# Optimization experiments

Hardware: AMD Instinct MI355X
Metric: run time of the kernel (lower is better)

Reference implementation:

```python
import jax, jax.numpy as jnp
import numpy as np

EMBED_DIM = 1024
NUM_HEADS = 16
HEAD_DIM = EMBED_DIM // NUM_HEADS
SEG_LENS = [1024, 2048, 4096]
DIL_RATIOS = [1, 2, 4]
NEG = -1e8  # lse fill value used by sparse_to_dense


def setup_inputs() -> dict:
    root = jax.random.key(0)
    ks = jax.random.split(root, 12)
    B, L, E = 1, 4096, EMBED_DIM
    s = 0.02
    return {
        "query": jax.random.normal(ks[0], (B, L, E), jnp.float32),
        "key": jax.random.normal(ks[1], (B, L, E), jnp.float32),
        "value": jax.random.normal(ks[2], (B, L, E), jnp.float32),
        "Wq": jax.random.normal(ks[3], (E, E), jnp.float32) * s,
        "bq": jnp.zeros((E,), jnp.float32),
        "Wk": jax.random.normal(ks[4], (E, E), jnp.float32) * s,
        "bk": jnp.zeros((E,), jnp.float32),
        "Wv": jax.random.normal(ks[5], (E, E), jnp.float32) * s,
        "bv": jnp.zeros((E,), jnp.float32),
        "Wo": jax.random.normal(ks[6], (E, E), jnp.float32) * s,
        "bo": jnp.zeros((E,), jnp.float32),
    }


def _branch(q, k, v, sl, dr, L):
    """One (segment_length, dilated_ratio) branch.
    q,k,v: (B, L, H, D). Returns dense out (B, H, L, D) and lse (B, H, L).
    """
    B = q.shape[0]
    H, D = NUM_HEADS, HEAD_DIM
    sl = min(sl, L)
    pad = (-L) % sl
    if pad:
        pw = ((0, 0), (0, pad), (0, 0), (0, 0))
        q, k, v = jnp.pad(q, pw), jnp.pad(k, pw), jnp.pad(v, pw)
    n = (L + pad) // sl  # segments
    qs = q.reshape(B * n, sl, H, D)
    ks = k.reshape(B * n, sl, H, D)
    vs = v.reshape(B * n, sl, H, D)
    # dense_to_sparse: head j (group r = j // (H//dr)) keeps positions i*dr + r
    hg = H // dr
    g = sl // dr
    grp = jnp.arange(H) // hg                      # (H,)
    pos = jnp.arange(g)[:, None] * dr + grp[None]  # (g, H) dense positions
    hidx = jnp.arange(H)[None, :]
    sp = lambda x: x[:, pos, hidx, :]              # (B*n, g, H, D)
    qd, kd, vd = sp(qs), sp(ks), sp(vs)
    # causal attention within each sparse segment (flash_attn semantics)
    scores = jnp.einsum('bqhd,bkhd->bhqk', qd, kd) * (D ** -0.5)
    mask = jnp.tril(jnp.ones((g, g), bool))
    scores = jnp.where(mask, scores, -jnp.inf)
    lse = jax.nn.logsumexp(scores, axis=-1)        # (B*n, H, g)
    o = jnp.einsum('bhqk,bkhd->bqhd', jnp.exp(scores - lse[..., None]), vd)
    # sparse_to_dense: scatter back onto dense positions, NEG elsewhere
    hcol = jnp.arange(H)[:, None]                  # (H,1)
    od = jnp.zeros((B * n, H, sl, D), o.dtype).at[:, hcol, pos.T].set(
        o.transpose(0, 2, 1, 3))
    ld = jnp.zeros((B * n, H, sl), lse.dtype).at[:, hcol, pos.T].set(lse)
    ld = jnp.where(ld == 0.0, NEG, ld)  # matches masked_fill_(lse == 0, -1e8)
    od = od.reshape(B, n, H, sl, D).transpose(0, 2, 1, 3, 4)
    od = od.reshape(B, H, n * sl, D)[:, :, :L]
    ld = ld.reshape(B, n, H, sl).transpose(0, 2, 1, 3).reshape(B, H, n * sl)[:, :, :L]
    return od, ld


def reference(query, key, value, Wq, bq, Wk, bk, Wv, bv, Wo, bo):
    B, L, E = query.shape
    H, D = NUM_HEADS, HEAD_DIM
    q = (query @ Wq.T + bq).reshape(B, L, H, D)
    k = (key @ Wk.T + bk).reshape(B, L, H, D)
    v = (value @ Wv.T + bv).reshape(B, L, H, D)
    outs, lses = [], []
    for sl, dr in zip(SEG_LENS, DIL_RATIOS):
        o, l = _branch(q, k, v, sl, dr, L)
        outs.append(o)
        lses.append(l)
    lse_all = jnp.stack(lses, 0)[..., None]        # (nb, B, H, L, 1)
    m = lse_all.max(0)
    w = jnp.exp(lse_all - m)
    w = w / w.sum(0)                               # softmax merge weights
    w = jax.lax.stop_gradient(w)                   # torch computes under no_grad
    out = sum(o * wi.astype(o.dtype) for o, wi in zip(outs, w))  # (B,H,L,D)
    out = out.transpose(0, 2, 1, 3).reshape(B, L, E)
    return out @ Wo.T + bo
```

## Files before the change

kernel.cpp:

```cpp
#include <hip/hip_runtime.h>
#include <math.h>


#define L_SEQ 4096
#define EDIM  1024
#define NH    16
#define HD    64
#define GLEN  1024

typedef __bf16 bf16;
typedef __bf16 bf16x8 __attribute__((ext_vector_type(8)));
typedef __bf16 bf16x4 __attribute__((ext_vector_type(4)));
typedef short  s16x4  __attribute__((ext_vector_type(4)));
typedef float  f32x4  __attribute__((ext_vector_type(4)));

template <bool B> struct Flag { static constexpr bool v = B; };

__device__ __forceinline__ void gload16(const bf16* g, bf16* l) {
  __builtin_amdgcn_global_load_lds(
      (__attribute__((address_space(1))) void*)(const_cast<bf16*>(g)),
      (__attribute__((address_space(3))) void*)(l),
      16, 0, 0);
}

__device__ __forceinline__ f32x4 mfma16x16x16_bf16(bf16x4 a, bf16x4 b, f32x4 c) {
#if defined(__HIP_DEVICE_COMPILE__)
  union { bf16x4 h; s16x4 s; } ua, ub;
  ua.h = a; ub.h = b;
  return __builtin_amdgcn_mfma_f32_16x16x16bf16_1k(ua.s, ub.s, c, 0, 0, 0);
#else
  (void)a; (void)b;
  return c;
#endif
}

__device__ __forceinline__ float fast_exp2(float x) {
#if __has_builtin(__builtin_amdgcn_exp2f)
  return __builtin_amdgcn_exp2f(x);
#else
  return __expf(x * 0.6931471805599453f);
#endif
}

__global__ __launch_bounds__(256) void cvt_kernel(
    const float* q, const float* k, const float* v,
    const float* wq, const float* wk, const float* wv, const float* wo,
    bf16* oq, bf16* ok, bf16* ov,
    bf16* owq, bf16* owk, bf16* owv, bf16* owo)
{
  const float* src; bf16* dst; int n;
  switch (blockIdx.y) {
    case 0: src = q;  dst = oq;  n = L_SEQ*EDIM; break;
    case 1: src = k;  dst = ok;  n = L_SEQ*EDIM; break;
    case 2: src = v;  dst = ov;  n = L_SEQ*EDIM; break;
    case 3: src = wq; dst = owq; n = EDIM*EDIM; break;
    case 4: src = wk; dst = owk; n = EDIM*EDIM; break;
    case 5: src = wv; dst = owv; n = EDIM*EDIM; break;
    default: src = wo; dst = owo; n = EDIM*EDIM; break;
  }
  int i = (blockIdx.x * 256 + threadIdx.x) * 8;
  if (i >= n) return;
  const float4* s4 = (const float4*)(src + i);
  float4 a = s4[0], b = s4[1];
  bf16x8 o = { (bf16)a.x, (bf16)a.y, (bf16)a.z, (bf16)a.w,
               (bf16)b.x, (bf16)b.y, (bf16)b.z, (bf16)b.w };
  *(bf16x8*)(dst + i) = o;
}

template <typename OutT>
__device__ __forceinline__ void gemm_body(const bf16* __restrict__ A,
                                          const bf16* __restrict__ W,
                                          const float* __restrict__ bias,
                                          OutT* __restrict__ C)
{
  constexpr int K = 1024;
  __shared__ __align__(16) bf16 lA[128 * 32];
  __shared__ __align__(16) bf16 lB[128 * 32];

  const int tid  = threadIdx.x;
  const int lane = tid & 63;
  const int w    = tid >> 6;
  const int quad = lane >> 4;
  const int l16  = lane & 15;
  const int wr   = w >> 1, wc = w & 1;
  const int ly = blockIdx.x * 4 + (blockIdx.y >> 3);
  const int lx = blockIdx.y & 7;
  const int row0 = ly * 128;
  const int col0 = lx * 128;

  f32x4 acc[4][4] = {};

  const int c0 = tid, c1 = tid + 256;
  const bf16* Ab0 = A + (size_t)(row0 + (c0 >> 2)) * K + (c0 & 3) * 8;
  const bf16* Ab1 = A + (size_t)(row0 + (c1 >> 2)) * K + (c1 & 3) * 8;
  const bf16* Bb0 = W + (size_t)(col0 + (c0 >> 2)) * K + (c0 & 3) * 8;
  const bf16* Bb1 = W + (size_t)(col0 + (c1 >> 2)) * K + (c1 & 3) * 8;
  bf16* lA0 = &lA[c0 * 8]; bf16* lA1 = &lA[c1 * 8];
  bf16* lB0 = &lB[c0 * 8]; bf16* lB1 = &lB[c1 * 8];

  for (int kt = 0; kt < K; kt += 32) {
    __syncthreads();
    gload16(Ab0 + kt, lA0);
    gload16(Ab1 + kt, lA1);
    gload16(Bb0 + kt, lB0);
    gload16(Bb1 + kt, lB1);
    __syncthreads();

    bf16x8 af[4], bfrag[4];
#pragma unroll
    for (int mi = 0; mi < 4; mi++)
      af[mi] = *(const bf16x8*)&lA[(wr * 64 + mi * 16 + l16) * 32 + quad * 8];
#pragma unroll
    for (int ni = 0; ni < 4; ni++)
      bfrag[ni] = *(const bf16x8*)&lB[(wc * 64 + ni * 16 + l16) * 32 + quad * 8];
#pragma unroll
    for (int mi = 0; mi < 4; mi++)
#pragma unroll
      for (int ni = 0; ni < 4; ni++)
        acc[mi][ni] = __builtin_amdgcn_mfma_f32_16x16x32_bf16(
            af[mi], bfrag[ni], acc[mi][ni], 0, 0, 0);
  }

#pragma unroll
  for (int mi = 0; mi < 4; mi++) {
#pragma unroll
    for (int ni = 0; ni < 4; ni++) {
      const int gcol = col0 + wc * 64 + ni * 16 + l16;
      const float bv = bias[gcol];
#pragma unroll
      for (int r = 0; r < 4; r++) {
        const int grow = row0 + wr * 64 + mi * 16 + quad * 4 + r;
        C[(size_t)grow * 1024 + gcol] = (OutT)(acc[mi][ni][r] + bv);
      }
    }
  }
}

__global__ __launch_bounds__(256) void gemm_qkv_kernel(
    const bf16* xq, const bf16* xk, const bf16* xv,
    const bf16* wq, const bf16* wk, const bf16* wv,
    const float* bq, const float* bk, const float* bv,
    bf16* q, bf16* k, bf16* v)
{
  const bf16 *A, *W; const float* bias; bf16* C;
  if (blockIdx.z == 0)      { A = xq; W = wq; bias = bq; C = q; }
  else if (blockIdx.z == 1) { A = xk; W = wk; bias = bk; C = k; }
  else                      { A = xv; W = wv; bias = bv; C = v; }
  gemm_body<bf16>(A, W, bias, C);
}

__global__ __launch_bounds__(256) void gemm_out_kernel(
    const bf16* A, const bf16* W, const float* bias, float* C)
{
  gemm_body<float>(A, W, bias, C);
}

__global__ __launch_bounds__(256) void vtrans_kernel(
    const bf16* __restrict__ v, bf16* vt0, bf16* vt1, bf16* vt2)
{
  __shared__ __align__(16) bf16 ltile[64 * 72];
  const int bid = blockIdx.x;
  int sl, dr, rem, shift; bf16* vt;
  if (bid < 1024)      { sl = 1024; dr = 1; rem = bid;        vt = vt0; shift = 4; }
  else if (bid < 1536) { sl = 2048; dr = 2; rem = bid - 1024; vt = vt1; shift = 3; }
  else                 { sl = 4096; dr = 4; rem = bid - 1536; vt = vt2; shift = 2; }
  const int ktile = rem & 15;
  const int h     = (rem >> 4) & 15;
  const int seg   = rem >> 8;
  const int grp   = h >> shift;
  const int segbase = seg * sl;
  const int tid = threadIdx.x;
  {
    const int i = tid >> 2, dc = tid & 3;
    const size_t p = (size_t)(segbase + (ktile * 64 + i) * dr + grp);
    const bf16* src = v + p * EDIM + h * 64 + dc * 16;
    *(uint4*)&ltile[i * 72 + dc * 16]     = *(const uint4*)(src);
    *(uint4*)&ltile[i * 72 + dc * 16 + 8] = *(const uint4*)(src + 8);
  }
  __syncthreads();
  {
    const int d = tid >> 2, kc = tid & 3;
    __align__(16) bf16 tmp[16];
#pragma unroll
    for (int j = 0; j < 16; j++) tmp[j] = ltile[(kc * 16 + j) * 72 + d];
    const int p2 = kc >> 1, half = kc & 1;
    bf16* dst = vt + ((size_t)(seg * NH + h) * 64 + d) * GLEN + ktile * 64
                   + p2 * 32 + half * 4;
#pragma unroll
    for (int q = 0; q < 4; q++) {
      bf16x4 piece = { tmp[q * 4 + 0], tmp[q * 4 + 1],
                       tmp[q * 4 + 2], tmp[q * 4 + 3] };
      *(bf16x4*)(dst + q * 8) = piece;
    }
  }
}

__global__ __launch_bounds__(256, 4) void attn_kernel(
    const bf16* __restrict__ qg, const bf16* __restrict__ kg,
    const bf16* vt0, const bf16* vt1, const bf16* vt2,
    bf16* o0, bf16* o1, bf16* o2,
    float* l0, float* l1, float* l2)
{
  __shared__ __align__(16) bf16 lK[2][64 * 64];
  __shared__ __align__(16) bf16 lV[2][64 * 64];

  const int bid0 = blockIdx.x;
  const int o = (bid0 & 7) * 112 + (bid0 >> 3);

  int sl, dr, rem, shift;
  const bf16* vt; bf16* ob; float* lseb;
  if (o < 512)      { sl = 1024; dr = 1; rem = o;       vt = vt0; ob = o0; lseb = l0; shift = 4; }
  else if (o < 768) { sl = 2048; dr = 2; rem = o - 512; vt = vt1; ob = o1; lseb = l1; shift = 3; }
  else              { sl = 4096; dr = 4; rem = o - 768; vt = vt2; ob = o2; lseb = l2; shift = 2; }
  const int j   = rem & 7;
  const int h   = (rem >> 3) & 15;
  const int seg = rem >> 7;
  const int qtA = 15 - j;
  const int qtB = j;
  const int grp = h >> shift;
  const int segbase = seg * sl;

  const int tid = threadIdx.x, lane = tid & 63, w = tid >> 6;
  const int quad = lane >> 4, l16 = lane & 15;
  const int rs8 = l16 & 7;

  auto loadq = [&](int qt, bf16x8& a0, bf16x8& a1) {
    const int qi = qt * 64 + w * 16 + l16;
    const size_t p = (size_t)(segbase + qi * dr + grp);
    const bf16* qp = qg + p * EDIM + h * 64 + quad * 8;
    a0 = *(const bf16x8*)(qp);
    a1 = *(const bf16x8*)(qp + 32);
  };
  bf16x8 qaA0, qaA1, qaB0, qaB1;
  loadq(qtA, qaA0, qaA1);
  loadq(qtB, qaB0, qaB1);

  f32x4 OA[4] = {}, OB[4] = {};
  float mA = -__builtin_inff(), lA_ = 0.f;
  float mB = -__builtin_inff(), lB_ = 0.f;

  const bf16* vbase = vt + (size_t)(seg * NH + h) * 64 * GLEN;
  const int c0 = tid, c1 = tid + 256;
  const int r0 = c0 >> 3, sw0 = ((c0 & 7) ^ (r0 & 7));
  const int r1 = c1 >> 3, sw1 = ((c1 & 7) ^ (r1 & 7));

  const bf16* kp0 = kg + (size_t)(segbase + r0 * dr + grp) * EDIM + h * 64 + sw0 * 8;
  const bf16* kp1 = kg + (size_t)(segbase + r1 * dr + grp) * EDIM + h * 64 + sw1 * 8;
  const bf16* vp0 = vbase + (size_t)r0 * GLEN + sw0 * 8;
  const bf16* vp1 = vbase + (size_t)r1 * GLEN + sw1 * 8;
  const size_t kstep = (size_t)64 * dr * EDIM;

  auto stage = [&](int buf) {
    gload16(kp0, &lK[buf][c0 * 8]);
    gload16(kp1, &lK[buf][c1 * 8]);
    gload16(vp0, &lV[buf][c0 * 8]);
    gload16(vp1, &lV[buf][c1 * 8]);
    kp0 += kstep; kp1 += kstep; vp0 += 64; vp1 += 64;
  };

  const float CS = 0.18033688011112042f;
  const float NEGINF = -__builtin_inff();
  const int qiA = qtA * 64 + w * 16 + l16;
  const int qiB = qtB * 64 + w * 16 + l16;

  const int kb0 = l16 * 64 + ((quad ^ rs8) * 8);
  const int kb1 = l16 * 64 + (((4 + quad) ^ rs8) * 8);
  const int vb0 = l16 * 64;

  auto comp = [&](auto hasB_, auto diagA_, auto diagB_, int kt) {
    constexpr bool HAS_B  = decltype(hasB_)::v;
    constexpr bool DIAG_A = decltype(diagA_)::v;
    constexpr bool DIAG_B = decltype(diagB_)::v;
    const bf16* bK = lK[kt & 1];
    const bf16* bV = lV[kt & 1];

    f32x4 sA[4], sB[4];
    __builtin_amdgcn_s_setprio(1);
#pragma unroll
    for (int t = 0; t < 4; t++) {
      const bool aA = !DIAG_A || t <= w;
      const bool aB = HAS_B && (!DIAG_B || t <= w);
      if (aA || aB) {
        bf16x8 ka0 = *(const bf16x8*)&bK[kb0 + t * 1024];
        bf16x8 ka1 = *(const bf16x8*)&bK[kb1 + t * 1024];
        if (aA) {
          sA[t] = f32x4{0.f, 0.f, 0.f, 0.f};
          sA[t] = __builtin_amdgcn_mfma_f32_16x16x32_bf16(ka0, qaA0, sA[t], 0, 0, 0);
          sA[t] = __builtin_amdgcn_mfma_f32_16x16x32_bf16(ka1, qaA1, sA[t], 0, 0, 0);
        }
        if (aB) {
          sB[t] = f32x4{0.f, 0.f, 0.f, 0.f};
          sB[t] = __builtin_amdgcn_mfma_f32_16x16x32_bf16(ka0, qaB0, sB[t], 0, 0, 0);
          sB[t] = __builtin_amdgcn_mfma_f32_16x16x32_bf16(ka1, qaB1, sB[t], 0, 0, 0);
        }
      }
    }
    __builtin_amdgcn_s_setprio(0);

    f32x4 mvA = {NEGINF, NEGINF, NEGINF, NEGINF};
    f32x4 mvB = {NEGINF, NEGINF, NEGINF, NEGINF};
#pragma unroll
    for (int t = 0; t < 4; t++) {
      if (!DIAG_A || t <= w) {
#pragma unroll
        for (int r = 0; r < 4; r++) {
          float sv = sA[t][r];
          if (DIAG_A) {
            const int kj = kt * 64 + t * 16 + quad * 4 + r;
            if (kj > qiA) sv = NEGINF;
          }
          sA[t][r] = sv;
          mvA[r] = fmaxf(mvA[r], sv);
        }
      }
      if (HAS_B && (!DIAG_B || t <= w)) {
#pragma unroll
        for (int r = 0; r < 4; r++) {
          float sv = sB[t][r];
          if (DIAG_B) {
            const int kj = kt * 64 + t * 16 + quad * 4 + r;
            if (kj > qiB) sv = NEGINF;
          }
          sB[t][r] = sv;
          mvB[r] = fmaxf(mvB[r], sv);
        }
      }
    }
    float mrA = fmaxf(fmaxf(mvA[0], mvA[1]), fmaxf(mvA[2], mvA[3]));
    float mrB = fmaxf(fmaxf(mvB[0], mvB[1]), fmaxf(mvB[2], mvB[3]));
    mrA = fmaxf(mrA, __shfl_xor(mrA, 16, 64));
    mrA = fmaxf(mrA, __shfl_xor(mrA, 32, 64));
    if constexpr (HAS_B) {
      mrB = fmaxf(mrB, __shfl_xor(mrB, 16, 64));
      mrB = fmaxf(mrB, __shfl_xor(mrB, 32, 64));
    }

    {
      const float mnew = fmaxf(mA, mrA * CS);
      if (!__all(mnew - mA <= 8.0f)) {
        const float alpha = fast_exp2(mA - mnew);
#pragma unroll
        for (int nf = 0; nf < 4; nf++)
#pragma unroll
          for (int r = 0; r < 4; r++) OA[nf][r] *= alpha;
        lA_ *= alpha;
        mA = mnew;
      }
    }
    if constexpr (HAS_B) {
      const float mnew = fmaxf(mB, mrB * CS);
      if (!__all(mnew - mB <= 8.0f)) {
        const float alpha = fast_exp2(mB - mnew);
#pragma unroll
        for (int nf = 0; nf < 4; nf++)
#pragma unroll
          for (int r = 0; r < 4; r++) OB[nf][r] *= alpha;
        lB_ *= alpha;
        mB = mnew;
      }
    }

    bf16x4 pbA[4], pbB[4];
    f32x4 rvA = {0.f, 0.f, 0.f, 0.f}, rvB = {0.f, 0.f, 0.f, 0.f};
#pragma unroll
    for (int t = 0; t < 4; t++) {
      if (!DIAG_A || t <= w) {
#pragma unroll
        for (int r = 0; r < 4; r++) {
          const float pv = fast_exp2(__builtin_fmaf(sA[t][r], CS, -mA));
          pbA[t][r] = (bf16)pv;
          rvA[r] += pv;
        }
      }
      if (HAS_B && (!DIAG_B || t <= w)) {
#pragma unroll
        for (int r = 0; r < 4; r++) {
          const float pv = fast_exp2(__builtin_fmaf(sB[t][r], CS, -mB));
          pbB[t][r] = (bf16)pv;
          rvB[r] += pv;
        }
      }
    }
    float rsA = (rvA[0] + rvA[1]) + (rvA[2] + rvA[3]);
    rsA += __shfl_xor(rsA, 16, 64);
    rsA += __shfl_xor(rsA, 32, 64);
    lA_ += rsA;
    if constexpr (HAS_B) {
      float rsB = (rvB[0] + rvB[1]) + (rvB[2] + rvB[3]);
      rsB += __shfl_xor(rsB, 16, 64);
      rsB += __shfl_xor(rsB, 32, 64);
      lB_ += rsB;
    }

    __builtin_amdgcn_s_setprio(1);
#pragma unroll
    for (int p2 = 0; p2 < 2; p2++) {
      const int t0 = 2 * p2, t1 = t0 + 1;
      const bool aA0 = !DIAG_A || t0 <= w;
      const bool aA1 = !DIAG_A || t1 <= w;
      const bool aB0 = HAS_B && (!DIAG_B || t0 <= w);
      const bool aB1 = HAS_B && (!DIAG_B || t1 <= w);
      if (aA0 || aA1 || aB0 || aB1) {
        const int cx = ((p2 * 4 + quad) ^ rs8) * 8;
#pragma unroll
        for (int nf = 0; nf < 4; nf++) {
          bf16x8 va8 = *(const bf16x8*)&bV[vb0 + nf * 1024 + cx];
          bf16x4 vlo = __builtin_shufflevector(va8, va8, 0, 1, 2, 3);
          bf16x4 vhi = __builtin_shufflevector(va8, va8, 4, 5, 6, 7);
          if (aA0) OA[nf] = mfma16x16x16_bf16(vlo, pbA[t0], OA[nf]);
          if (aA1) OA[nf] = mfma16x16x16_bf16(vhi, pbA[t1], OA[nf]);
          if (aB0) OB[nf] = mfma16x16x16_bf16(vlo, pbB[t0], OB[nf]);
          if (aB1) OB[nf] = mfma16x16x16_bf16(vhi, pbB[t1], OB[nf]);
        }
      }
    }
    __builtin_amdgcn_s_setprio(0);
  };

  stage(0);
  int kt = 0;
  for (; kt < qtB; kt++) {
    __syncthreads();
    stage((kt + 1) & 1);
    comp(Flag<true>{}, Flag<false>{}, Flag<false>{}, kt);
  }
  __syncthreads();
  stage((kt + 1) & 1);
  comp(Flag<true>{}, Flag<false>{}, Flag<true>{}, kt);
  kt++;
  for (; kt < qtA; kt++) {
    __syncthreads();
    stage((kt + 1) & 1);
    comp(Flag<false>{}, Flag<false>{}, Flag<false>{}, kt);
  }
  __syncthreads();
  comp(Flag<false>{}, Flag<true>{}, Flag<false>{}, kt);

  auto epilogue = [&](const f32x4 (&Oa)[4], float m_r, float l_r, int qt) {
    const int qi = qt * 64 + w * 16 + l16;
    const float linv = 1.0f / l_r;
    const int pdense = segbase + qi * dr + grp;
    bf16* orow = ob + (size_t)pdense * EDIM + h * 64;
#pragma unroll
    for (int nf = 0; nf < 4; nf++) {
      bf16x4 ov;
#pragma unroll
      for (int r = 0; r < 4; r++) ov[r] = (bf16)(Oa[nf][r] * linv);
      *(bf16x4*)(orow + nf * 16 + quad * 4) = ov;
    }
    if (quad == 0)
      lseb[h * L_SEQ + pdense] = m_r * 0.6931471805599453f + __logf(l_r);
  };
  epilogue(OA, mA, lA_, qtA);
  epilogue(OB, mB, lB_, qtB);
}

__global__ __launch_bounds__(256) void merge_kernel(
    const bf16* __restrict__ o0, const bf16* __restrict__ o1, const bf16* __restrict__ o2,
    const float* __restrict__ l0, const float* __restrict__ l1, const float* __restrict__ l2,
    bf16* __restrict__ merged)
{
  const int idx = blockIdx.x * 256 + threadIdx.x;
  const int dc = idx & 7;
  const int h  = (idx >> 3) & 15;
  const int p  = idx >> 7;
  const bool c1 = ((p & 1) == (h >> 3));
  const bool c2 = ((p & 3) == (h >> 2));
  const float s0 = l0[h * L_SEQ + p];
  const float s1 = c1 ? l1[h * L_SEQ + p] : -__builtin_inff();
  const float s2 = c2 ? l2[h * L_SEQ + p] : -__builtin_inff();
  const float mx = fmaxf(s0, fmaxf(s1, s2));
  float w0 = __expf(s0 - mx);
  float w1 = c1 ? __expf(s1 - mx) : 0.f;
  float w2 = c2 ? __expf(s2 - mx) : 0.f;
  const float inv = 1.0f / (w0 + w1 + w2);
  w0 *= inv; w1 *= inv; w2 *= inv;

  const size_t off = (size_t)p * EDIM + h * 64 + dc * 8;
  float acc[8];
  bf16x8 a0 = *(const bf16x8*)(o0 + off);
#pragma unroll
  for (int j = 0; j < 8; j++) acc[j] = w0 * (float)a0[j];
  if (c1) {
    bf16x8 a1 = *(const bf16x8*)(o1 + off);
#pragma unroll
    for (int j = 0; j < 8; j++) acc[j] += w1 * (float)a1[j];
  }
  if (c2) {
    bf16x8 a2 = *(const bf16x8*)(o2 + off);
#pragma unroll
    for (int j = 0; j < 8; j++) acc[j] += w2 * (float)a2[j];
  }
  bf16x8 r;
#pragma unroll
  for (int j = 0; j < 8; j++) r[j] = (bf16)acc[j];
  *(bf16x8*)(merged + off) = r;
}

extern "C" void kernel_launch(void* const* d_in, const int* in_sizes, int n_in,
                              void* d_out, int out_size, void* d_ws, size_t ws_size,
                              hipStream_t stream)
{
  (void)in_sizes; (void)n_in; (void)out_size; (void)ws_size;
  const float* query = (const float*)d_in[0];
  const float* key   = (const float*)d_in[1];
  const float* value = (const float*)d_in[2];
  const float* Wq = (const float*)d_in[3];
  const float* bq = (const float*)d_in[4];
  const float* Wk = (const float*)d_in[5];
  const float* bk = (const float*)d_in[6];
  const float* Wv = (const float*)d_in[7];
  const float* bv = (const float*)d_in[8];
  const float* Wo = (const float*)d_in[9];
  const float* bo = (const float*)d_in[10];

  char* base = (char*)d_ws;
  size_t off = 0;
  auto take = [&](size_t nbytes) -> char* {
    char* p = base + off;
    off += (nbytes + 255) & ~(size_t)255;
    return p;
  };
  const size_t LE2 = (size_t)L_SEQ * EDIM * 2;
  const size_t EE2 = (size_t)EDIM * EDIM * 2;
  bf16* xq  = (bf16*)take(LE2);
  bf16* xk  = (bf16*)take(LE2);
  bf16* xv  = (bf16*)take(LE2);
  bf16* wqb = (bf16*)take(EE2);
  bf16* wkb = (bf16*)take(EE2);
  bf16* wvb = (bf16*)take(EE2);
  bf16* wob = (bf16*)take(EE2);
  bf16* qb  = (bf16*)take(LE2);
  bf16* kb  = (bf16*)take(LE2);
  bf16* vb  = (bf16*)take(LE2);
  bf16* vt0 = (bf16*)take((size_t)4 * NH * HD * GLEN * 2);
  bf16* vt1 = (bf16*)take((size_t)2 * NH * HD * GLEN * 2);
  bf16* vt2 = (bf16*)take((size_t)1 * NH * HD * GLEN * 2);
  float* lse0 = (float*)take((size_t)NH * L_SEQ * 4);
  float* lse1 = (float*)take((size_t)NH * L_SEQ * 4);
  float* lse2 = (float*)take((size_t)NH * L_SEQ * 4);
  bf16* merged = (bf16*)take(LE2);
  bf16* o0 = xq; bf16* o1 = xk; bf16* o2 = xv;

  dim3 blk(256);
  cvt_kernel<<<dim3(2048, 7), blk, 0, stream>>>(
      query, key, value, Wq, Wk, Wv, Wo, xq, xk, xv, wqb, wkb, wvb, wob);
  gemm_qkv_kernel<<<dim3(8, 32, 3), blk, 0, stream>>>(
      xq, xk, xv, wqb, wkb, wvb, bq, bk, bv, qb, kb, vb);
  vtrans_kernel<<<dim3(1792), blk, 0, stream>>>(vb, vt0, vt1, vt2);
  attn_kernel<<<dim3(896), blk, 0, stream>>>(
      qb, kb, vt0, vt1, vt2, o0, o1, o2, lse0, lse1, lse2);
  merge_kernel<<<dim3(2048), blk, 0, stream>>>(
      o0, o1, o2, lse0, lse1, lse2, merged);
  gemm_out_kernel<<<dim3(8, 32), blk, 0, stream>>>(merged, wob, bo, (float*)d_out);
}
```

Measured before the change: 227.2 us.

## Fuse fp32-to-bf16 activation conversion into QKV GEMM and compute row sums via MFMA

The QKV GEMM now reads fp32 activations directly, converting them to bf16 in registers and prefetching the next K-tile into registers before writing it to LDS. This removes the separate conversion pass over the three large input tensors and its bf16 round trip through memory. In the attention kernel, the softmax row-sum is accumulated with an MFMA against a ones vector instead of VALU adds and cross-lane shuffles. The s_setprio hints are also removed. The trade-off is extra MFMA issue in attention, and in the GEMM a register-staged A path that replaces the async global-to-LDS load.

```diff
diff --git a/kernel.cpp b/kernel.cpp
--- a/kernel.cpp
+++ b/kernel.cpp
@@ -43,23 +43,17 @@
 }
 
 __global__ __launch_bounds__(256) void cvt_kernel(
-    const float* q, const float* k, const float* v,
     const float* wq, const float* wk, const float* wv, const float* wo,
-    bf16* oq, bf16* ok, bf16* ov,
     bf16* owq, bf16* owk, bf16* owv, bf16* owo)
 {
-  const float* src; bf16* dst; int n;
+  const float* src; bf16* dst;
   switch (blockIdx.y) {
-    case 0: src = q;  dst = oq;  n = L_SEQ*EDIM; break;
-    case 1: src = k;  dst = ok;  n = L_SEQ*EDIM; break;
-    case 2: src = v;  dst = ov;  n = L_SEQ*EDIM; break;
-    case 3: src = wq; dst = owq; n = EDIM*EDIM; break;
-    case 4: src = wk; dst = owk; n = EDIM*EDIM; break;
-    case 5: src = wv; dst = owv; n = EDIM*EDIM; break;
-    default: src = wo; dst = owo; n = EDIM*EDIM; break;
-  }
-  int i = (blockIdx.x * 256 + threadIdx.x) * 8;
-  if (i >= n) return;
+    case 0: src = wq; dst = owq; break;
+    case 1: src = wk; dst = owk; break;
+    case 2: src = wv; dst = owv; break;
+    default: src = wo; dst = owo; break;
+  }
+  const int i = (blockIdx.x * 256 + threadIdx.x) * 8;
   const float4* s4 = (const float4*)(src + i);
   float4 a = s4[0], b = s4[1];
   bf16x8 o = { (bf16)a.x, (bf16)a.y, (bf16)a.z, (bf16)a.w,
@@ -67,8 +61,8 @@
   *(bf16x8*)(dst + i) = o;
 }
 
-template <typename OutT>
-__device__ __forceinline__ void gemm_body(const bf16* __restrict__ A,
+template <typename OutT, bool AF32>
+__device__ __forceinline__ void gemm_body(const void* __restrict__ Ap,
                                           const bf16* __restrict__ W,
                                           const float* __restrict__ bias,
                                           OutT* __restrict__ C)
@@ -91,20 +85,48 @@
   f32x4 acc[4][4] = {};
 
   const int c0 = tid, c1 = tid + 256;
-  const bf16* Ab0 = A + (size_t)(row0 + (c0 >> 2)) * K + (c0 & 3) * 8;
-  const bf16* Ab1 = A + (size_t)(row0 + (c1 >> 2)) * K + (c1 & 3) * 8;
   const bf16* Bb0 = W + (size_t)(col0 + (c0 >> 2)) * K + (c0 & 3) * 8;
   const bf16* Bb1 = W + (size_t)(col0 + (c1 >> 2)) * K + (c1 & 3) * 8;
-  bf16* lA0 = &lA[c0 * 8]; bf16* lA1 = &lA[c1 * 8];
-  bf16* lB0 = &lB[c0 * 8]; bf16* lB1 = &lB[c1 * 8];
+
+  const bf16* Ab0 = nullptr; const bf16* Ab1 = nullptr;
+  const float* Af0 = nullptr; const float* Af1 = nullptr;
+  float4 ar0, ar1, ar2, ar3;
+  if constexpr (AF32) {
+    const float* Af = (const float*)Ap;
+    Af0 = Af + (size_t)(row0 + (c0 >> 2)) * K + (c0 & 3) * 8;
+    Af1 = Af + (size_t)(row0 + (c1 >> 2)) * K + (c1 & 3) * 8;
+    ar0 = *(const float4*)(Af0); ar1 = *(const float4*)(Af0 + 4);
+    ar2 = *(const float4*)(Af1); ar3 = *(const float4*)(Af1 + 4);
+    Af0 += 32; Af1 += 32;
+  } else {
+    const bf16* Ab = (const bf16*)Ap;
+    Ab0 = Ab + (size_t)(row0 + (c0 >> 2)) * K + (c0 & 3) * 8;
+    Ab1 = Ab + (size_t)(row0 + (c1 >> 2)) * K + (c1 & 3) * 8;
+  }
 
   for (int kt = 0; kt < K; kt += 32) {
     __syncthreads();
-    gload16(Ab0 + kt, lA0);
-    gload16(Ab1 + kt, lA1);
-    gload16(Bb0 + kt, lB0);
-    gload16(Bb1 + kt, lB1);
+    if constexpr (AF32) {
+      bf16x8 wa = { (bf16)ar0.x, (bf16)ar0.y, (bf16)ar0.z, (bf16)ar0.w,
+                    (bf16)ar1.x, (bf16)ar1.y, (bf16)ar1.z, (bf16)ar1.w };
+      bf16x8 wb = { (bf16)ar2.x, (bf16)ar2.y, (bf16)ar2.z, (bf16)ar2.w,
+                    (bf16)ar3.x, (bf16)ar3.y, (bf16)ar3.z, (bf16)ar3.w };
+      *(bf16x8*)&lA[c0 * 8] = wa;
+      *(bf16x8*)&lA[c1 * 8] = wb;
+    } else {
+      gload16(Ab0 + kt, &lA[c0 * 8]);
+      gload16(Ab1 + kt, &lA[c1 * 8]);
+    }
+    gload16(Bb0 + kt, &lB[c0 * 8]);
+    gload16(Bb1 + kt, &lB[c1 * 8]);
     __syncthreads();
+    if constexpr (AF32) {
+      if (kt + 32 < K) {
+        ar0 = *(const float4*)(Af0); ar1 = *(const float4*)(Af0 + 4);
+        ar2 = *(const float4*)(Af1); ar3 = *(const float4*)(Af1 + 4);
+        Af0 += 32; Af1 += 32;
+      }
+    }
 
     bf16x8 af[4], bfrag[4];
 #pragma unroll
@@ -137,22 +159,22 @@
 }
 
 __global__ __launch_bounds__(256) void gemm_qkv_kernel(
-    const bf16* xq, const bf16* xk, const bf16* xv,
+    const float* q, const float* k, const float* v,
     const bf16* wq, const bf16* wk, const bf16* wv,
     const float* bq, const float* bk, const float* bv,
-    bf16* q, bf16* k, bf16* v)
-{
-  const bf16 *A, *W; const float* bias; bf16* C;
-  if (blockIdx.z == 0)      { A = xq; W = wq; bias = bq; C = q; }
-  else if (blockIdx.z == 1) { A = xk; W = wk; bias = bk; C = k; }
-  else                      { A = xv; W = wv; bias = bv; C = v; }
-  gemm_body<bf16>(A, W, bias, C);
+    bf16* qo, bf16* ko, bf16* vo)
+{
+  const float *A, *bias; const bf16* W; bf16* C;
+  if (blockIdx.z == 0)      { A = q; W = wq; bias = bq; C = qo; }
+  else if (blockIdx.z == 1) { A = k; W = wk; bias = bk; C = ko; }
+  else                      { A = v; W = wv; bias = bv; C = vo; }
+  gemm_body<bf16, true>(A, W, bias, C);
 }
 
 __global__ __launch_bounds__(256) void gemm_out_kernel(
     const bf16* A, const bf16* W, const float* bias, float* C)
 {
-  gemm_body<float>(A, W, bias, C);
+  gemm_body<float, false>(A, W, bias, C);
 }
 
 __global__ __launch_bounds__(256) void vtrans_kernel(
@@ -236,8 +258,11 @@
   loadq(qtB, qaB0, qaB1);
 
   f32x4 OA[4] = {}, OB[4] = {};
-  float mA = -__builtin_inff(), lA_ = 0.f;
-  float mB = -__builtin_inff(), lB_ = 0.f;
+  f32x4 lsA = {0.f, 0.f, 0.f, 0.f};
+  f32x4 lsB = {0.f, 0.f, 0.f, 0.f};
+  float mA = -__builtin_inff();
+  float mB = -__builtin_inff();
+  const bf16x4 ONES = { (bf16)1.f, (bf16)1.f, (bf16)1.f, (bf16)1.f };
 
   const bf16* vbase = vt + (size_t)(seg * NH + h) * 64 * GLEN;
   const int c0 = tid, c1 = tid + 256;
@@ -275,7 +300,6 @@
     const bf16* bV = lV[kt & 1];
 
     f32x4 sA[4], sB[4];
-    __builtin_amdgcn_s_setprio(1);
 #pragma unroll
     for (int t = 0; t < 4; t++) {
       const bool aA = !DIAG_A || t <= w;
@@ -295,7 +319,6 @@
         }
       }
     }
-    __builtin_amdgcn_s_setprio(0);
 
     f32x4 mvA = {NEGINF, NEGINF, NEGINF, NEGINF};
     f32x4 mvB = {NEGINF, NEGINF, NEGINF, NEGINF};
@@ -343,7 +366,8 @@
         for (int nf = 0; nf < 4; nf++)
 #pragma unroll
           for (int r = 0; r < 4; r++) OA[nf][r] *= alpha;
-        lA_ *= alpha;
+#pragma unroll
+        for (int r = 0; r < 4; r++) lsA[r] *= alpha;
         mA = mnew;
       }
     }
@@ -355,44 +379,27 @@
         for (int nf = 0; nf < 4; nf++)
 #pragma unroll
           for (int r = 0; r < 4; r++) OB[nf][r] *= alpha;
-        lB_ *= alpha;
+#pragma unroll
+        for (int r = 0; r < 4; r++) lsB[r] *= alpha;
         mB = mnew;
       }
     }
 
     bf16x4 pbA[4], pbB[4];
-    f32x4 rvA = {0.f, 0.f, 0.f, 0.f}, rvB = {0.f, 0.f, 0.f, 0.f};
 #pragma unroll
     for (int t = 0; t < 4; t++) {
       if (!DIAG_A || t <= w) {
 #pragma unroll
-        for (int r = 0; r < 4; r++) {
-          const float pv = fast_exp2(__builtin_fmaf(sA[t][r], CS, -mA));
-          pbA[t][r] = (bf16)pv;
-          rvA[r] += pv;
-        }
+        for (int r = 0; r < 4; r++)
+          pbA[t][r] = (bf16)fast_exp2(__builtin_fmaf(sA[t][r], CS, -mA));
       }
       if (HAS_B && (!DIAG_B || t <= w)) {
 #pragma unroll
-        for (int r = 0; r < 4; r++) {
-          const float pv = fast_exp2(__builtin_fmaf(sB[t][r], CS, -mB));
-          pbB[t][r] = (bf16)pv;
-          rvB[r] += pv;
-        }
-      }
-    }
-    float rsA = (rvA[0] + rvA[1]) + (rvA[2] + rvA[3]);
-    rsA += __shfl_xor(rsA, 16, 64);
-    rsA += __shfl_xor(rsA, 32, 64);
-    lA_ += rsA;
-    if constexpr (HAS_B) {
-      float rsB = (rvB[0] + rvB[1]) + (rvB[2] + rvB[3]);
-      rsB += __shfl_xor(rsB, 16, 64);
-      rsB += __shfl_xor(rsB, 32, 64);
-      lB_ += rsB;
-    }
-
-    __builtin_amdgcn_s_setprio(1);
+        for (int r = 0; r < 4; r++)
+          pbB[t][r] = (bf16)fast_exp2(__builtin_fmaf(sB[t][r], CS, -mB));
+      }
+    }
+
 #pragma unroll
     for (int p2 = 0; p2 < 2; p2++) {
       const int t0 = 2 * p2, t1 = t0 + 1;
@@ -412,9 +419,12 @@
           if (aB0) OB[nf] = mfma16x16x16_bf16(vlo, pbB[t0], OB[nf]);
           if (aB1) OB[nf] = mfma16x16x16_bf16(vhi, pbB[t1], OB[nf]);
         }
-      }
-    }
-    __builtin_amdgcn_s_setprio(0);
+        if (aA0) lsA = mfma16x16x16_bf16(ONES, pbA[t0], lsA);
+        if (aA1) lsA = mfma16x16x16_bf16(ONES, pbA[t1], lsA);
+        if (aB0) lsB = mfma16x16x16_bf16(ONES, pbB[t0], lsB);
+        if (aB1) lsB = mfma16x16x16_bf16(ONES, pbB[t1], lsB);
+      }
+    }
   };
 
   stage(0);
@@ -451,8 +461,8 @@
     if (quad == 0)
       lseb[h * L_SEQ + pdense] = m_r * 0.6931471805599453f + __logf(l_r);
   };
-  epilogue(OA, mA, lA_, qtA);
-  epilogue(OB, mB, lB_, qtB);
+  epilogue(OA, mA, lsA[0], qtA);
+  epilogue(OB, mB, lsB[0], qtB);
 }
 
 __global__ __launch_bounds__(256) void merge_kernel(
@@ -523,9 +533,6 @@
   };
   const size_t LE2 = (size_t)L_SEQ * EDIM * 2;
   const size_t EE2 = (size_t)EDIM * EDIM * 2;
-  bf16* xq  = (bf16*)take(LE2);
-  bf16* xk  = (bf16*)take(LE2);
-  bf16* xv  = (bf16*)take(LE2);
   bf16* wqb = (bf16*)take(EE2);
   bf16* wkb = (bf16*)take(EE2);
   bf16* wvb = (bf16*)take(EE2);
@@ -533,6 +540,9 @@
   bf16* qb  = (bf16*)take(LE2);
   bf16* kb  = (bf16*)take(LE2);
   bf16* vb  = (bf16*)take(LE2);
+  bf16* o0  = (bf16*)take(LE2);
+  bf16* o1  = (bf16*)take(LE2);
+  bf16* o2  = (bf16*)take(LE2);
   bf16* vt0 = (bf16*)take((size_t)4 * NH * HD * GLEN * 2);
   bf16* vt1 = (bf16*)take((size_t)2 * NH * HD * GLEN * 2);
   bf16* vt2 = (bf16*)take((size_t)1 * NH * HD * GLEN * 2);
@@ -540,13 +550,12 @@
   float* lse1 = (float*)take((size_t)NH * L_SEQ * 4);
   float* lse2 = (float*)take((size_t)NH * L_SEQ * 4);
   bf16* merged = (bf16*)take(LE2);
-  bf16* o0 = xq; bf16* o1 = xk; bf16* o2 = xv;
 
   dim3 blk(256);
-  cvt_kernel<<<dim3(2048, 7), blk, 0, stream>>>(
-      query, key, value, Wq, Wk, Wv, Wo, xq, xk, xv, wqb, wkb, wvb, wob);
+  cvt_kernel<<<dim3(512, 4), blk, 0, stream>>>(
+      Wq, Wk, Wv, Wo, wqb, wkb, wvb, wob);
   gemm_qkv_kernel<<<dim3(8, 32, 3), blk, 0, stream>>>(
-      xq, xk, xv, wqb, wkb, wvb, bq, bk, bv, qb, kb, vb);
+      query, key, value, wqb, wkb, wvb, bq, bk, bv, qb, kb, vb);
   vtrans_kernel<<<dim3(1792), blk, 0, stream>>>(vb, vt0, vt1, vt2);
   attn_kernel<<<dim3(896), blk, 0, stream>>>(
       qb, kb, vt0, vt1, vt2, o0, o1, o2, lse0, lse1, lse2);
```

Result: no change. 229.2 us (+0.9%).

## Double-buffer GEMM LDS tiles and compute softmax row sums with MFMA

Applied to the files above, without the earlier changes.

The projection GEMM now uses two LDS buffers, loading the next K-slice while the current one is multiplied, with one barrier per iteration instead of two. In the attention kernel the per-row softmax denominator is no longer built from scalar adds plus cross-lane shuffles. It is accumulated by MFMA against a vector of ones, reusing the bf16 probabilities, and the s_setprio hints are removed. This trades shuffle and VALU work for extra MFMA instructions and doubles GEMM LDS use, which may lower occupancy. The row sum now comes from bf16-rounded probabilities, which slightly changes numerics.

```diff
diff --git a/kernel.cpp b/kernel.cpp
--- a/kernel.cpp
+++ b/kernel.cpp
@@ -74,8 +74,8 @@
                                           OutT* __restrict__ C)
 {
   constexpr int K = 1024;
-  __shared__ __align__(16) bf16 lA[128 * 32];
-  __shared__ __align__(16) bf16 lB[128 * 32];
+  __shared__ __align__(16) bf16 lA[2][128 * 32];
+  __shared__ __align__(16) bf16 lB[2][128 * 32];
 
   const int tid  = threadIdx.x;
   const int lane = tid & 63;
@@ -95,30 +95,36 @@
   const bf16* Ab1 = A + (size_t)(row0 + (c1 >> 2)) * K + (c1 & 3) * 8;
   const bf16* Bb0 = W + (size_t)(col0 + (c0 >> 2)) * K + (c0 & 3) * 8;
   const bf16* Bb1 = W + (size_t)(col0 + (c1 >> 2)) * K + (c1 & 3) * 8;
-  bf16* lA0 = &lA[c0 * 8]; bf16* lA1 = &lA[c1 * 8];
-  bf16* lB0 = &lB[c0 * 8]; bf16* lB1 = &lB[c1 * 8];
-
-  for (int kt = 0; kt < K; kt += 32) {
-    __syncthreads();
-    gload16(Ab0 + kt, lA0);
-    gload16(Ab1 + kt, lA1);
-    gload16(Bb0 + kt, lB0);
-    gload16(Bb1 + kt, lB1);
-    __syncthreads();
+
+  auto stage = [&](int kt, int buf) {
+    gload16(Ab0 + kt, &lA[buf][c0 * 8]);
+    gload16(Ab1 + kt, &lA[buf][c1 * 8]);
+    gload16(Bb0 + kt, &lB[buf][c0 * 8]);
+    gload16(Bb1 + kt, &lB[buf][c1 * 8]);
+  };
+
+  stage(0, 0);
+  __syncthreads();
+
+  for (int t = 0; t < 32; ++t) {
+    const int cur = t & 1;
+    if (t < 31) stage((t + 1) * 32, cur ^ 1);
 
     bf16x8 af[4], bfrag[4];
 #pragma unroll
     for (int mi = 0; mi < 4; mi++)
-      af[mi] = *(const bf16x8*)&lA[(wr * 64 + mi * 16 + l16) * 32 + quad * 8];
+      af[mi] = *(const bf16x8*)&lA[cur][(wr * 64 + mi * 16 + l16) * 32 + quad * 8];
 #pragma unroll
     for (int ni = 0; ni < 4; ni++)
-      bfrag[ni] = *(const bf16x8*)&lB[(wc * 64 + ni * 16 + l16) * 32 + quad * 8];
+      bfrag[ni] = *(const bf16x8*)&lB[cur][(wc * 64 + ni * 16 + l16) * 32 + quad * 8];
 #pragma unroll
     for (int mi = 0; mi < 4; mi++)
 #pragma unroll
       for (int ni = 0; ni < 4; ni++)
         acc[mi][ni] = __builtin_amdgcn_mfma_f32_16x16x32_bf16(
             af[mi], bfrag[ni], acc[mi][ni], 0, 0, 0);
+
+    __syncthreads();
   }
 
 #pragma unroll
@@ -236,8 +242,11 @@
   loadq(qtB, qaB0, qaB1);
 
   f32x4 OA[4] = {}, OB[4] = {};
-  float mA = -__builtin_inff(), lA_ = 0.f;
-  float mB = -__builtin_inff(), lB_ = 0.f;
+  f32x4 lsA = {0.f, 0.f, 0.f, 0.f};
+  f32x4 lsB = {0.f, 0.f, 0.f, 0.f};
+  float mA = -__builtin_inff();
+  float mB = -__builtin_inff();
+  const bf16x4 ONES = { (bf16)1.f, (bf16)1.f, (bf16)1.f, (bf16)1.f };
 
   const bf16* vbase = vt + (size_t)(seg * NH + h) * 64 * GLEN;
   const int c0 = tid, c1 = tid + 256;
@@ -275,7 +284,6 @@
     const bf16* bV = lV[kt & 1];
 
     f32x4 sA[4], sB[4];
-    __builtin_amdgcn_s_setprio(1);
 #pragma unroll
     for (int t = 0; t < 4; t++) {
       const bool aA = !DIAG_A || t <= w;
@@ -295,7 +303,6 @@
         }
       }
     }
-    __builtin_amdgcn_s_setprio(0);
 
     f32x4 mvA = {NEGINF, NEGINF, NEGINF, NEGINF};
     f32x4 mvB = {NEGINF, NEGINF, NEGINF, NEGINF};
@@ -343,7 +350,8 @@
         for (int nf = 0; nf < 4; nf++)
 #pragma unroll
           for (int r = 0; r < 4; r++) OA[nf][r] *= alpha;
-        lA_ *= alpha;
+#pragma unroll
+        for (int r = 0; r < 4; r++) lsA[r] *= alpha;
         mA = mnew;
       }
     }
@@ -355,44 +363,27 @@
         for (int nf = 0; nf < 4; nf++)
 #pragma unroll
           for (int r = 0; r < 4; r++) OB[nf][r] *= alpha;
-        lB_ *= alpha;
+#pragma unroll
+        for (int r = 0; r < 4; r++) lsB[r] *= alpha;
         mB = mnew;
       }
     }
 
     bf16x4 pbA[4], pbB[4];
-    f32x4 rvA = {0.f, 0.f, 0.f, 0.f}, rvB = {0.f, 0.f, 0.f, 0.f};
 #pragma unroll
     for (int t = 0; t < 4; t++) {
       if (!DIAG_A || t <= w) {
 #pragma unroll
-        for (int r = 0; r < 4; r++) {
-          const float pv = fast_exp2(__builtin_fmaf(sA[t][r], CS, -mA));
-          pbA[t][r] = (bf16)pv;
-          rvA[r] += pv;
-        }
+        for (int r = 0; r < 4; r++)
+          pbA[t][r] = (bf16)fast_exp2(__builtin_fmaf(sA[t][r], CS, -mA));
       }
       if (HAS_B && (!DIAG_B || t <= w)) {
 #pragma unroll
-        for (int r = 0; r < 4; r++) {
-          const float pv = fast_exp2(__builtin_fmaf(sB[t][r], CS, -mB));
-          pbB[t][r] = (bf16)pv;
-          rvB[r] += pv;
-        }
-      }
-    }
-    float rsA = (rvA[0] + rvA[1]) + (rvA[2] + rvA[3]);
-    rsA += __shfl_xor(rsA, 16, 64);
-    rsA += __shfl_xor(rsA, 32, 64);
-    lA_ += rsA;
-    if constexpr (HAS_B) {
-      float rsB = (rvB[0] + rvB[1]) + (rvB[2] + rvB[3]);
-      rsB += __shfl_xor(rsB, 16, 64);
-      rsB += __shfl_xor(rsB, 32, 64);
-      lB_ += rsB;
-    }
-
-    __builtin_amdgcn_s_setprio(1);
+        for (int r = 0; r < 4; r++)
+          pbB[t][r] = (bf16)fast_exp2(__builtin_fmaf(sB[t][r], CS, -mB));
+      }
+    }
+
 #pragma unroll
     for (int p2 = 0; p2 < 2; p2++) {
       const int t0 = 2 * p2, t1 = t0 + 1;
@@ -412,9 +403,12 @@
           if (aB0) OB[nf] = mfma16x16x16_bf16(vlo, pbB[t0], OB[nf]);
           if (aB1) OB[nf] = mfma16x16x16_bf16(vhi, pbB[t1], OB[nf]);
         }
-      }
-    }
-    __builtin_amdgcn_s_setprio(0);
+        if (aA0) lsA = mfma16x16x16_bf16(ONES, pbA[t0], lsA);
+        if (aA1) lsA = mfma16x16x16_bf16(ONES, pbA[t1], lsA);
+        if (aB0) lsB = mfma16x16x16_bf16(ONES, pbB[t0], lsB);
+        if (aB1) lsB = mfma16x16x16_bf16(ONES, pbB[t1], lsB);
+      }
+    }
   };
 
   stage(0);
@@ -451,8 +445,8 @@
     if (quad == 0)
       lseb[h * L_SEQ + pdense] = m_r * 0.6931471805599453f + __logf(l_r);
   };
-  epilogue(OA, mA, lA_, qtA);
-  epilogue(OB, mB, lB_, qtB);
+  epilogue(OA, mA, lsA[0], qtA);
+  epilogue(OB, mB, lsB[0], qtB);
 }
 
 __global__ __launch_bounds__(256) void merge_kernel(
```

Measured after the change: 228.8 us. Within noise of the previous version (+0.7%).
